# Optimization experiments

Hardware: AMD Instinct MI355X
Metric: run time of the kernel (lower is better)

## Reference

```python
import jax, jax.numpy as jnp
import numpy as np

D_MODEL = 1024
NUM_HEADS = 16
PERIOD_LEN = 4096
HEAD_DIM = D_MODEL // NUM_HEADS


def setup_inputs() -> dict:
    key = jax.random.key(0)
    ks = jax.random.split(key, 10)
    B, S, D = 2, 2048, D_MODEL
    scale = 1.0 / np.sqrt(D)
    inp = {
        "x": jax.random.normal(ks[0], (B, S, D), dtype=jnp.float32),
        "wq": jax.random.normal(ks[1], (D, D), dtype=jnp.float32) * scale,
        "bq": jnp.zeros((D,), dtype=jnp.float32),
        "wk": jax.random.normal(ks[2], (D, D), dtype=jnp.float32) * scale,
        "bk": jnp.zeros((D,), dtype=jnp.float32),
        "wv": jax.random.normal(ks[3], (D, D), dtype=jnp.float32) * scale,
        "bv": jnp.zeros((D,), dtype=jnp.float32),
        "wo": jax.random.normal(ks[4], (D, D), dtype=jnp.float32) * scale,
        "bo": jnp.zeros((D,), dtype=jnp.float32),
        # original init is zeros; use small randn so bias path is non-trivial
        "rel_bias": jax.random.normal(ks[5], (PERIOD_LEN, NUM_HEADS), dtype=jnp.float32) * 0.02,
    }
    return inp


def reference(x, wq, bq, wk, bk, wv, bv, wo, bo, rel_bias):
    B, S, D = x.shape
    H, Hd = NUM_HEADS, HEAD_DIM
    q = (x @ wq + bq).reshape(B, S, H, Hd).transpose(0, 2, 1, 3)  # [B,H,S,Hd]
    k = (x @ wk + bk).reshape(B, S, H, Hd).transpose(0, 2, 1, 3)
    v = (x @ wv + bv).reshape(B, S, H, Hd).transpose(0, 2, 1, 3)
    scores = jnp.einsum('bhqd,bhkd->bhqk', q, k) / jnp.sqrt(jnp.float32(Hd))
    if S <= PERIOD_LEN:
        pos = jnp.arange(S)
        circ = (pos[:, None] - pos[None, :]) % PERIOD_LEN  # [S,S]
        bias = rel_bias[circ]                               # [S,S,H]
        scores = scores + bias.transpose(2, 0, 1)[None]     # [1,H,S,S]
    attn = jax.nn.softmax(scores, axis=-1)
    out = jnp.einsum('bhqk,bhkd->bhqd', attn, v)
    out = out.transpose(0, 2, 1, 3).reshape(B, S, D)
    return out @ wo + bo
```

## Files before the change

kernel.cpp:

```cpp
#include <hip/hip_runtime.h>
#include <hip/hip_bf16.h>

#define D_MODEL 1024
#define NHEADS  16
#define HEADD   64
#define SEQ     2048
#define PERIOD  4096
#define LOG2E   1.44269504088896340736f

typedef __attribute__((ext_vector_type(4)))  float f32x4;
typedef __attribute__((ext_vector_type(16))) float f32x16;
typedef __attribute__((ext_vector_type(4)))  float fvec4;
typedef __attribute__((ext_vector_type(8)))  short s16x8;
typedef __attribute__((ext_vector_type(4)))  short s16x4;
typedef __attribute__((ext_vector_type(2)))  int   i32x2;
typedef __attribute__((ext_vector_type(4)))  int   i32x4;

__device__ __forceinline__ short bf16_bits(float f) {
    union { float f; unsigned u; } v; v.f = f;
    unsigned r = v.u + 0x7FFFu + ((v.u >> 16) & 1u);
    return (short)(r >> 16);
}

__device__ __forceinline__ int cvt_pk_bf16(float a, float b) {
    int r;
    asm("v_cvt_pk_bf16_f32 %0, %1, %2" : "=v"(r) : "v"(a), "v"(b));
    return r;
}

__device__ __forceinline__ float bf16_to_f32(short s) {
    return __int_as_float(((int)(unsigned short)s) << 16);
}

__device__ __forceinline__ float exp2_hw(float x) {
    float r;
    asm("v_exp_f32 %0, %1" : "=v"(r) : "v"(x));
    return r;
}

__device__ __forceinline__ void gload_lds16(const void* g, void* l) {
    __builtin_amdgcn_global_load_lds(
        (const __attribute__((address_space(1))) void*)g,
        (__attribute__((address_space(3))) void*)l, 16, 0, 0);
}

__global__ void cvt_x(const float* __restrict__ x, short* __restrict__ xb) {
    int i = blockIdx.x * blockDim.x + threadIdx.x;
    fvec4 v = ((const fvec4*)x)[i];
    s16x4 o;
    o.x = bf16_bits(v.x); o.y = bf16_bits(v.y);
    o.z = bf16_bits(v.z); o.w = bf16_bits(v.w);
    ((s16x4*)xb)[i] = o;
}

__global__ void transpose_w4(const float* __restrict__ wq, const float* __restrict__ wk,
                             const float* __restrict__ wv, const float* __restrict__ wo,
                             short* __restrict__ wqkv, short* __restrict__ wot) {
    __shared__ float tile[64][65];
    int wsel = blockIdx.y;
    const float* src = wsel == 0 ? wq : (wsel == 1 ? wk : (wsel == 2 ? wv : wo));
    short* dst = wsel < 3 ? wqkv + wsel * 1024 * 1024 : wot;
    int bx = blockIdx.x & 15, by = blockIdx.x >> 4;
    int n0 = bx * 64, k0 = by * 64;
    int t = threadIdx.x;
    int cr = t >> 4;
    int cc = (t & 15) * 4;
    for (int i = 0; i < 4; ++i) {
        int row = cr + i * 16;
        fvec4 v = *(const fvec4*)&src[(k0 + row) * D_MODEL + n0 + cc];
        tile[row][cc+0] = v.x; tile[row][cc+1] = v.y;
        tile[row][cc+2] = v.z; tile[row][cc+3] = v.w;
    }
    __syncthreads();
    for (int i = 0; i < 4; ++i) {
        int row = cr + i * 16;
        s16x4 o;
        o.x = bf16_bits(tile[cc+0][row]);
        o.y = bf16_bits(tile[cc+1][row]);
        o.z = bf16_bits(tile[cc+2][row]);
        o.w = bf16_bits(tile[cc+3][row]);
        *(s16x4*)&dst[(n0 + row) * D_MODEL + k0 + cc] = o;
    }
}

__global__ void transpose_v(const short* __restrict__ vb, short* __restrict__ vt) {
    __shared__ short tile[64][80];
    int bh = blockIdx.y, st = blockIdx.x;
    int b = bh >> 4, h = bh & 15;
    int s0 = st * 64;
    int t = threadIdx.x;
    int row = t >> 3, ch = t & 7;
    for (int i = 0; i < 2; ++i) {
        int r = row + i * 32;
        *(s16x8*)&tile[r][ch * 8] =
            *(const s16x8*)&vb[(b * SEQ + s0 + r) * D_MODEL + h * HEADD + ch * 8];
    }
    __syncthreads();
    for (int i = 0; i < 2; ++i) {
        int d = row + i * 32;
        s16x8 o;
        #pragma unroll
        for (int j = 0; j < 8; ++j) o[j] = tile[ch * 8 + j][d];
        *(s16x8*)&vt[(b * D_MODEL + h * HEADD + d) * SEQ + s0 + ch * 8] = o;
    }
}

__global__ void build_biasq(const float* __restrict__ rb, f32x4* __restrict__ bq4) {
    int id = blockIdx.x * 256 + threadIdx.x;
    int h = id >> 12, a = id & 4095;
    f32x4 v;
    #pragma unroll
    for (int j = 0; j < 4; ++j)
        v[j] = rb[((a + j) & (PERIOD - 1)) * NHEADS + h] * LOG2E - 16.0f;
    bq4[id] = v;
}

__global__ __launch_bounds__(256, 3) void gemm_qkv(
    const short* __restrict__ A, const short* __restrict__ Bt,
    const float* __restrict__ biasq, const float* __restrict__ biask,
    const float* __restrict__ biasv,
    short* __restrict__ qb, short* __restrict__ kb, short* __restrict__ vb)
{
    __shared__ short As[2][128 * 64];
    __shared__ short Bs[2][64 * 64];
    int tid = threadIdx.x;
    int lane = tid & 63, wid = tid >> 6;
    int ln = lane & 15, g = lane >> 4;
    int wr = (wid >> 1) * 64, wc = (wid & 1) * 32;

    int bid = blockIdx.x;
    int xcd = bid & 7, slot = bid >> 3;
    int mb = xcd * 4 + (slot / 48);
    int nb = slot % 48;
    int m0 = mb * 128, n0 = nb * 64;

    int wsel = n0 >> 10;
    const float* bias = wsel == 0 ? biasq : (wsel == 1 ? biask : biasv);
    short* dst = wsel == 0 ? qb : (wsel == 1 ? kb : vb);
    float osc = wsel == 0 ? (0.125f * LOG2E) : 1.0f;
    int ncol0 = n0 & 1023;

    f32x4 acc[4][2] = {};

    auto STAGE = [&](int kt, int bi) {
        #pragma unroll
        for (int i = 0; i < 4; ++i) {
            int idx = i * 256 + tid;
            int row = idx >> 3, ch = idx & 7;
            int gch = ch ^ (row & 7);
            gload_lds16(&A[(m0 + row) * 1024 + kt + gch * 8],
                        (char*)&As[bi][0] + (i * 256 + wid * 64) * 16);
        }
        #pragma unroll
        for (int i = 0; i < 2; ++i) {
            int idx = i * 256 + tid;
            int row = idx >> 3, ch = idx & 7;
            int gch = ch ^ (row & 7);
            gload_lds16(&Bt[(n0 + row) * 1024 + kt + gch * 8],
                        (char*)&Bs[bi][0] + (i * 256 + wid * 64) * 16);
        }
    };

    STAGE(0, 0);
    __syncthreads();

    for (int kt = 0; kt < 16; ++kt) {
        int bi = kt & 1;
        if (kt < 15) STAGE((kt + 1) * 64, bi ^ 1);

        s16x8 af[4][2], bfr[2][2];
        #pragma unroll
        for (int m = 0; m < 4; ++m) {
            int row = wr + m * 16 + ln;
            #pragma unroll
            for (int kc = 0; kc < 2; ++kc)
                af[m][kc] = *(const s16x8*)&As[bi][row * 64 + (((kc * 4 + g) ^ (row & 7)) * 8)];
        }
        #pragma unroll
        for (int n = 0; n < 2; ++n) {
            int row = wc + n * 16 + ln;
            #pragma unroll
            for (int kc = 0; kc < 2; ++kc)
                bfr[n][kc] = *(const s16x8*)&Bs[bi][row * 64 + (((kc * 4 + g) ^ (row & 7)) * 8)];
        }
        #pragma unroll
        for (int kc = 0; kc < 2; ++kc)
            #pragma unroll
            for (int m = 0; m < 4; ++m)
                #pragma unroll
                for (int n = 0; n < 2; ++n)
                    acc[m][n] = __builtin_amdgcn_mfma_f32_16x16x32_bf16(af[m][kc], bfr[n][kc], acc[m][n], 0, 0, 0);

        __syncthreads();
    }

    #pragma unroll
    for (int m = 0; m < 4; ++m) {
        int gr0 = m0 + wr + m * 16 + g * 4;
        #pragma unroll
        for (int n = 0; n < 2; ++n) {
            int gc = ncol0 + wc + n * 16 + ln;
            float bvv = bias[gc];
            #pragma unroll
            for (int r = 0; r < 4; ++r)
                dst[(gr0 + r) * 1024 + gc] = bf16_bits((acc[m][n][r] + bvv) * osc);
        }
    }
}

template<int MODE>
__global__ __launch_bounds__(256) void gemm_bias(
    const short* __restrict__ A, const short* __restrict__ Bt,
    const float* __restrict__ bias, void* __restrict__ Cout)
{
    __shared__ short As[2][128 * 64];
    __shared__ short Bs[2][64 * 64];
    int tid = threadIdx.x;
    int lane = tid & 63, wid = tid >> 6;
    int ln = lane & 15, g = lane >> 4;
    int wr = (wid >> 1) * 64, wc = (wid & 1) * 32;

    int bid = blockIdx.x;
    int xcd = bid & 7, slot = bid >> 3;
    int mb = xcd * 4 + (slot >> 4);
    int nb = slot & 15;
    int m0 = mb * 128, n0 = nb * 64;

    f32x4 acc[4][2] = {};

    auto STAGE = [&](int kt, int bi) {
        #pragma unroll
        for (int i = 0; i < 4; ++i) {
            int idx = i * 256 + tid;
            int row = idx >> 3, ch = idx & 7;
            int gch = ch ^ (row & 7);
            gload_lds16(&A[(m0 + row) * 1024 + kt + gch * 8],
                        (char*)&As[bi][0] + (i * 256 + wid * 64) * 16);
        }
        #pragma unroll
        for (int i = 0; i < 2; ++i) {
            int idx = i * 256 + tid;
            int row = idx >> 3, ch = idx & 7;
            int gch = ch ^ (row & 7);
            gload_lds16(&Bt[(n0 + row) * 1024 + kt + gch * 8],
                        (char*)&Bs[bi][0] + (i * 256 + wid * 64) * 16);
        }
    };

    STAGE(0, 0);
    __syncthreads();

    for (int kt = 0; kt < 16; ++kt) {
        int bi = kt & 1;
        if (kt < 15) STAGE((kt + 1) * 64, bi ^ 1);

        s16x8 af[4][2], bfr[2][2];
        #pragma unroll
        for (int m = 0; m < 4; ++m) {
            int row = wr + m * 16 + ln;
            #pragma unroll
            for (int kc = 0; kc < 2; ++kc)
                af[m][kc] = *(const s16x8*)&As[bi][row * 64 + (((kc * 4 + g) ^ (row & 7)) * 8)];
        }
        #pragma unroll
        for (int n = 0; n < 2; ++n) {
            int row = wc + n * 16 + ln;
            #pragma unroll
            for (int kc = 0; kc < 2; ++kc)
                bfr[n][kc] = *(const s16x8*)&Bs[bi][row * 64 + (((kc * 4 + g) ^ (row & 7)) * 8)];
        }
        #pragma unroll
        for (int kc = 0; kc < 2; ++kc)
            #pragma unroll
            for (int m = 0; m < 4; ++m)
                #pragma unroll
                for (int n = 0; n < 2; ++n)
                    acc[m][n] = __builtin_amdgcn_mfma_f32_16x16x32_bf16(af[m][kc], bfr[n][kc], acc[m][n], 0, 0, 0);

        __syncthreads();
    }

    #pragma unroll
    for (int m = 0; m < 4; ++m) {
        int gr0 = m0 + wr + m * 16 + g * 4;
        #pragma unroll
        for (int n = 0; n < 2; ++n) {
            int gc = n0 + wc + n * 16 + ln;
            float bv = bias[gc];
            #pragma unroll
            for (int r = 0; r < 4; ++r) {
                int gr = gr0 + r;
                float v = acc[m][n][r] + bv;
                if (MODE == 0)      ((short*)Cout)[gr * 1024 + gc] = bf16_bits(v * (0.125f * LOG2E));
                else if (MODE == 1) ((short*)Cout)[gr * 1024 + gc] = bf16_bits(v);
                else                ((float*)Cout)[gr * 1024 + gc] = v;
            }
        }
    }
}

__global__ __launch_bounds__(256, 2) void attn_partial(
    const short* __restrict__ qb,
    const short* __restrict__ kb,
    const short* __restrict__ vt,
    const f32x4* __restrict__ biasq,
    short* __restrict__ po,
    float* __restrict__ pl)
{
    __shared__ short KV[2][2][64 * 64];

    int tid = threadIdx.x;
    int lane = tid & 63;
    int wid = tid >> 6;
    int l31 = lane & 31, hi = lane >> 5;

    int bid = blockIdx.x;
    int xcd = bid & 7, slot = bid >> 3;
    int hb = xcd * 4 + (slot >> 5);
    int qt = (slot >> 1) & 15;
    int half = slot & 1;
    int h = hb & 15, b = hb >> 4;
    int q0 = qt * 128 + wid * 32;
    int qrow = q0 + l31;
    int kbase = half * 1024;

    s16x8 aq[4];
    #pragma unroll
    for (int kk = 0; kk < 4; ++kk)
        aq[kk] = *(const s16x8*)&qb[(b * SEQ + qrow) * D_MODEL + h * HEADD + kk * 16 + hi * 8];

    const f32x4* bq = biasq + h * PERIOD;

    float lrow = 0.f;
    f32x16 ot[2] = {};

    auto STAGE = [&](int k0, int bi) {
        #pragma unroll
        for (int i = 0; i < 2; ++i) {
            int idx = i * 256 + tid;
            int row = idx >> 3, ch = idx & 7;
            int gch = ch ^ ((row & 7) ^ ((row >> 3) & 3));
            gload_lds16(&kb[(b * SEQ + k0 + row) * D_MODEL + h * HEADD + gch * 8],
                        (char*)&KV[bi][0][0] + (i * 256 + wid * 64) * 16);
            gload_lds16(&vt[(b * D_MODEL + h * HEADD + row) * SEQ + k0 + gch * 8],
                        (char*)&KV[bi][1][0] + (i * 256 + wid * 64) * 16);
        }
    };

    STAGE(kbase, 0);
    __syncthreads();

    for (int kt = 0; kt < 16; ++kt) {
        int k0 = kbase + kt * 64;
        int bi = kt & 1;
        if (kt < 15) STAGE(k0 + 64, bi ^ 1);

        f32x4 bv[2][4];
        #pragma unroll
        for (int kt32 = 0; kt32 < 2; ++kt32)
            #pragma unroll
            for (int rq = 0; rq < 4; ++rq) {
                int kq = k0 + kt32 * 32 + rq * 8 + hi * 4;
                bv[kt32][rq] = bq[(qrow - kq - 3) & (PERIOD - 1)];
            }

        f32x16 s[2];
        const short* Ksp = &KV[bi][0][0];
        const short* Vsp = &KV[bi][1][0];
        __builtin_amdgcn_s_setprio(1);
        #pragma unroll
        for (int kt32 = 0; kt32 < 2; ++kt32) {
            f32x16 acc = {};
            int rowK = kt32 * 32 + l31;
            int swz = (rowK & 7) ^ ((rowK >> 3) & 3);
            #pragma unroll
            for (int kk = 0; kk < 4; ++kk) {
                s16x8 kf = *(const s16x8*)&Ksp[rowK * 64 + (((2 * kk + hi) ^ swz) * 8)];
                acc = __builtin_amdgcn_mfma_f32_32x32x16_bf16(kf, aq[kk], acc, 0, 0, 0);
            }
            s[kt32] = acc;
        }
        __builtin_amdgcn_s_setprio(0);

        #pragma unroll
        for (int kt32 = 0; kt32 < 2; ++kt32)
            #pragma unroll
            for (int rq = 0; rq < 4; ++rq) {
                s[kt32][rq * 4 + 0] = exp2_hw(s[kt32][rq * 4 + 0] + bv[kt32][rq][3]);
                s[kt32][rq * 4 + 1] = exp2_hw(s[kt32][rq * 4 + 1] + bv[kt32][rq][2]);
                s[kt32][rq * 4 + 2] = exp2_hw(s[kt32][rq * 4 + 2] + bv[kt32][rq][1]);
                s[kt32][rq * 4 + 3] = exp2_hw(s[kt32][rq * 4 + 3] + bv[kt32][rq][0]);
            }

        float sm[16];
        #pragma unroll
        for (int t = 0; t < 16; ++t) sm[t] = s[0][t] + s[1][t];
        #pragma unroll
        for (int t = 0; t < 8; ++t) sm[t] += sm[t + 8];
        #pragma unroll
        for (int t = 0; t < 4; ++t) sm[t] += sm[t + 4];
        float psum = (sm[0] + sm[1]) + (sm[2] + sm[3]);
        {
            i32x2 r = __builtin_amdgcn_permlane32_swap(__float_as_int(psum), __float_as_int(psum), false, false);
            psum = __int_as_float(r[0]) + __int_as_float(r[1]);
        }
        lrow += psum;

        #pragma unroll
        for (int kt32 = 0; kt32 < 2; ++kt32) {
            int pk[8];
            #pragma unroll
            for (int i = 0; i < 8; ++i)
                pk[i] = cvt_pk_bf16(s[kt32][2 * i], s[kt32][2 * i + 1]);
            #pragma unroll
            for (int ks = 0; ks < 2; ++ks) {
                int a0 = pk[ks * 4 + 0], a1 = pk[ks * 4 + 1];
                int b0 = pk[ks * 4 + 2], b1 = pk[ks * 4 + 3];
                i32x2 r0 = __builtin_amdgcn_permlane32_swap(a0, b0, false, false);
                i32x2 r1 = __builtin_amdgcn_permlane32_swap(a1, b1, false, false);
                i32x4 wi;
                wi[0] = r0[0];
                wi[1] = r1[0];
                wi[2] = r0[1];
                wi[3] = r1[1];
                s16x8 pb = __builtin_bit_cast(s16x8, wi);
                __builtin_amdgcn_s_setprio(1);
                #pragma unroll
                for (int dd = 0; dd < 2; ++dd) {
                    int rowV = dd * 32 + l31;
                    int swzV = (rowV & 7) ^ ((rowV >> 3) & 3);
                    int chV = kt32 * 4 + ks * 2 + hi;
                    s16x8 vf = *(const s16x8*)&Vsp[rowV * 64 + ((chV ^ swzV) * 8)];
                    ot[dd] = __builtin_amdgcn_mfma_f32_32x32x16_bf16(vf, pb, ot[dd], 0, 0, 0);
                }
                __builtin_amdgcn_s_setprio(0);
            }
        }

        __syncthreads();
    }

    short* poH = po + half * (4096 * 1024);
    int obase = (b * SEQ + qrow) * D_MODEL + h * HEADD;
    #pragma unroll
    for (int dd = 0; dd < 2; ++dd)
        #pragma unroll
        for (int rq = 0; rq < 4; ++rq) {
            i32x2 st;
            st[0] = cvt_pk_bf16(ot[dd][rq * 4 + 0], ot[dd][rq * 4 + 1]);
            st[1] = cvt_pk_bf16(ot[dd][rq * 4 + 2], ot[dd][rq * 4 + 3]);
            *(i32x2*)&poH[obase + dd * 32 + rq * 8 + hi * 4] = st;
        }
    if (hi == 0)
        pl[half * (4096 * 16) + (b * SEQ + qrow) * 16 + h] = lrow;
}

__global__ __launch_bounds__(256) void attn_merge(
    const short* __restrict__ po, const float* __restrict__ pl,
    short* __restrict__ ao)
{
    int idx = blockIdx.x * 256 + threadIdx.x;
    int base = idx * 8;
    int row = base >> 10, col = base & 1023, h = col >> 6;
    float l = pl[row * 16 + h] + pl[4096 * 16 + row * 16 + h];
    float inv = 1.0f / l;
    s16x8 a = *(const s16x8*)&po[row * 1024 + col];
    s16x8 c = *(const s16x8*)&po[4096 * 1024 + row * 1024 + col];
    float v[8];
    #pragma unroll
    for (int j = 0; j < 8; ++j)
        v[j] = (bf16_to_f32(a[j]) + bf16_to_f32(c[j])) * inv;
    i32x4 o;
    o[0] = cvt_pk_bf16(v[0], v[1]);
    o[1] = cvt_pk_bf16(v[2], v[3]);
    o[2] = cvt_pk_bf16(v[4], v[5]);
    o[3] = cvt_pk_bf16(v[6], v[7]);
    *(i32x4*)&ao[base] = o;
}

extern "C" void kernel_launch(void* const* d_in, const int* in_sizes, int n_in,
                              void* d_out, int out_size, void* d_ws, size_t ws_size,
                              hipStream_t stream) {
    const float* x  = (const float*)d_in[0];
    const float* wq = (const float*)d_in[1];
    const float* bq = (const float*)d_in[2];
    const float* wk = (const float*)d_in[3];
    const float* bk = (const float*)d_in[4];
    const float* wv = (const float*)d_in[5];
    const float* bv = (const float*)d_in[6];
    const float* wo = (const float*)d_in[7];
    const float* bo = (const float*)d_in[8];
    const float* rb = (const float*)d_in[9];

    char* ws = (char*)d_ws;
    short* xb   = (short*)(ws);
    short* wqkv = (short*)(ws + (8u  << 20));
    short* wot  = (short*)(ws + (14u << 20));
    short* qb   = (short*)(ws + (16u << 20));
    short* kb   = (short*)(ws + (24u << 20));
    short* vb   = (short*)(ws + (32u << 20));
    short* vt   = (short*)(ws + (40u << 20));
    f32x4* bqt  = (f32x4*)(ws + (32u << 20));
    short* po   = (short*)(ws + (48u << 20));
    float* pl   = (float*)(ws + (64u << 20));
    short* ao   = xb;

    cvt_x<<<4096, 256, 0, stream>>>(x, xb);
    transpose_w4<<<dim3(256, 4), 256, 0, stream>>>(wq, wk, wv, wo, wqkv, wot);

    gemm_qkv<<<1536, 256, 0, stream>>>(xb, wqkv, bq, bk, bv, qb, kb, vb);
    transpose_v<<<dim3(32, 32), 256, 0, stream>>>(vb, vt);
    build_biasq<<<256, 256, 0, stream>>>(rb, bqt);

    attn_partial<<<1024, 256, 0, stream>>>(qb, kb, vt, bqt, po, pl);
    attn_merge<<<2048, 256, 0, stream>>>(po, pl, ao);

    gemm_bias<3><<<512, 256, 0, stream>>>(ao, wot, bo, (float*)d_out);
}
```

Before: 134.0 us.

## Merge prep kernels into one launch and write V transposed from QKV GEMM

Folds the x conversion, the weight transposes and the rel-bias table build into a single block-indexed prep kernel, removing three separate launches. The QKV GEMM epilogue now writes V directly in transposed [B, D, S] layout with packed bf16 stores, which removes the transpose_v kernel and its extra round trip through memory. The transposed V stores are 8-byte writes strided by sequence length, so they may coalesce less well than the row-major stores. The bias table now lives in the workspace slot that V used to occupy.

Measured after the change: 127.3 us. 1.05x faster.

```diff
diff --git a/kernel.cpp b/kernel.cpp
--- a/kernel.cpp
+++ b/kernel.cpp
@@ -44,82 +44,64 @@
         (__attribute__((address_space(3))) void*)l, 16, 0, 0);
 }
 
-__global__ void cvt_x(const float* __restrict__ x, short* __restrict__ xb) {
-    int i = blockIdx.x * blockDim.x + threadIdx.x;
-    fvec4 v = ((const fvec4*)x)[i];
-    s16x4 o;
-    o.x = bf16_bits(v.x); o.y = bf16_bits(v.y);
-    o.z = bf16_bits(v.z); o.w = bf16_bits(v.w);
-    ((s16x4*)xb)[i] = o;
-}
-
-__global__ void transpose_w4(const float* __restrict__ wq, const float* __restrict__ wk,
-                             const float* __restrict__ wv, const float* __restrict__ wo,
-                             short* __restrict__ wqkv, short* __restrict__ wot) {
+__global__ void prep_all(const float* __restrict__ x,
+                         const float* __restrict__ wq, const float* __restrict__ wk,
+                         const float* __restrict__ wv, const float* __restrict__ wo,
+                         const float* __restrict__ rb,
+                         short* __restrict__ xb, short* __restrict__ wqkv,
+                         short* __restrict__ wot, f32x4* __restrict__ bq4) {
     __shared__ float tile[64][65];
-    int wsel = blockIdx.y;
-    const float* src = wsel == 0 ? wq : (wsel == 1 ? wk : (wsel == 2 ? wv : wo));
-    short* dst = wsel < 3 ? wqkv + wsel * 1024 * 1024 : wot;
-    int bx = blockIdx.x & 15, by = blockIdx.x >> 4;
-    int n0 = bx * 64, k0 = by * 64;
+    int bid = blockIdx.x;
     int t = threadIdx.x;
-    int cr = t >> 4;
-    int cc = (t & 15) * 4;
-    for (int i = 0; i < 4; ++i) {
-        int row = cr + i * 16;
-        fvec4 v = *(const fvec4*)&src[(k0 + row) * D_MODEL + n0 + cc];
-        tile[row][cc+0] = v.x; tile[row][cc+1] = v.y;
-        tile[row][cc+2] = v.z; tile[row][cc+3] = v.w;
+    if (bid < 4096) {
+        int i = bid * 256 + t;
+        fvec4 v = ((const fvec4*)x)[i];
+        s16x4 o;
+        o.x = bf16_bits(v.x); o.y = bf16_bits(v.y);
+        o.z = bf16_bits(v.z); o.w = bf16_bits(v.w);
+        ((s16x4*)xb)[i] = o;
+    } else if (bid < 5120) {
+        int b2 = bid - 4096;
+        int wsel = b2 >> 8;
+        int bxy = b2 & 255;
+        const float* src = wsel == 0 ? wq : (wsel == 1 ? wk : (wsel == 2 ? wv : wo));
+        short* dst = wsel < 3 ? wqkv + wsel * 1024 * 1024 : wot;
+        int bx = bxy & 15, by = bxy >> 4;
+        int n0 = bx * 64, k0 = by * 64;
+        int cr = t >> 4;
+        int cc = (t & 15) * 4;
+        for (int i = 0; i < 4; ++i) {
+            int row = cr + i * 16;
+            fvec4 v = *(const fvec4*)&src[(k0 + row) * D_MODEL + n0 + cc];
+            tile[row][cc+0] = v.x; tile[row][cc+1] = v.y;
+            tile[row][cc+2] = v.z; tile[row][cc+3] = v.w;
+        }
+        __syncthreads();
+        for (int i = 0; i < 4; ++i) {
+            int row = cr + i * 16;
+            s16x4 o;
+            o.x = bf16_bits(tile[cc+0][row]);
+            o.y = bf16_bits(tile[cc+1][row]);
+            o.z = bf16_bits(tile[cc+2][row]);
+            o.w = bf16_bits(tile[cc+3][row]);
+            *(s16x4*)&dst[(n0 + row) * D_MODEL + k0 + cc] = o;
+        }
+    } else {
+        int id = (bid - 5120) * 256 + t;
+        int h = id >> 12, a = id & 4095;
+        f32x4 v;
+        #pragma unroll
+        for (int j = 0; j < 4; ++j)
+            v[j] = rb[((a + j) & (PERIOD - 1)) * NHEADS + h] * LOG2E - 16.0f;
+        bq4[id] = v;
     }
-    __syncthreads();
-    for (int i = 0; i < 4; ++i) {
-        int row = cr + i * 16;
-        s16x4 o;
-        o.x = bf16_bits(tile[cc+0][row]);
-        o.y = bf16_bits(tile[cc+1][row]);
-        o.z = bf16_bits(tile[cc+2][row]);
-        o.w = bf16_bits(tile[cc+3][row]);
-        *(s16x4*)&dst[(n0 + row) * D_MODEL + k0 + cc] = o;
-    }
-}
-
-__global__ void transpose_v(const short* __restrict__ vb, short* __restrict__ vt) {
-    __shared__ short tile[64][80];
-    int bh = blockIdx.y, st = blockIdx.x;
-    int b = bh >> 4, h = bh & 15;
-    int s0 = st * 64;
-    int t = threadIdx.x;
-    int row = t >> 3, ch = t & 7;
-    for (int i = 0; i < 2; ++i) {
-        int r = row + i * 32;
-        *(s16x8*)&tile[r][ch * 8] =
-            *(const s16x8*)&vb[(b * SEQ + s0 + r) * D_MODEL + h * HEADD + ch * 8];
-    }
-    __syncthreads();
-    for (int i = 0; i < 2; ++i) {
-        int d = row + i * 32;
-        s16x8 o;
-        #pragma unroll
-        for (int j = 0; j < 8; ++j) o[j] = tile[ch * 8 + j][d];
-        *(s16x8*)&vt[(b * D_MODEL + h * HEADD + d) * SEQ + s0 + ch * 8] = o;
-    }
-}
-
-__global__ void build_biasq(const float* __restrict__ rb, f32x4* __restrict__ bq4) {
-    int id = blockIdx.x * 256 + threadIdx.x;
-    int h = id >> 12, a = id & 4095;
-    f32x4 v;
-    #pragma unroll
-    for (int j = 0; j < 4; ++j)
-        v[j] = rb[((a + j) & (PERIOD - 1)) * NHEADS + h] * LOG2E - 16.0f;
-    bq4[id] = v;
 }
 
 __global__ __launch_bounds__(256, 3) void gemm_qkv(
     const short* __restrict__ A, const short* __restrict__ Bt,
     const float* __restrict__ biasq, const float* __restrict__ biask,
     const float* __restrict__ biasv,
-    short* __restrict__ qb, short* __restrict__ kb, short* __restrict__ vb)
+    short* __restrict__ qb, short* __restrict__ kb, short* __restrict__ vt)
 {
     __shared__ short As[2][128 * 64];
     __shared__ short Bs[2][64 * 64];
@@ -136,7 +118,6 @@
 
     int wsel = n0 >> 10;
     const float* bias = wsel == 0 ? biasq : (wsel == 1 ? biask : biasv);
-    short* dst = wsel == 0 ? qb : (wsel == 1 ? kb : vb);
     float osc = wsel == 0 ? (0.125f * LOG2E) : 1.0f;
     int ncol0 = n0 & 1023;
 
@@ -194,16 +175,34 @@
         __syncthreads();
     }
 
-    #pragma unroll
-    for (int m = 0; m < 4; ++m) {
-        int gr0 = m0 + wr + m * 16 + g * 4;
-        #pragma unroll
-        for (int n = 0; n < 2; ++n) {
-            int gc = ncol0 + wc + n * 16 + ln;
-            float bvv = bias[gc];
-            #pragma unroll
-            for (int r = 0; r < 4; ++r)
-                dst[(gr0 + r) * 1024 + gc] = bf16_bits((acc[m][n][r] + bvv) * osc);
+    if (wsel == 2) {
+        #pragma unroll
+        for (int m = 0; m < 4; ++m) {
+            int gr0 = m0 + wr + m * 16 + g * 4;
+            int b = gr0 >> 11, s0 = gr0 & 2047;
+            #pragma unroll
+            for (int n = 0; n < 2; ++n) {
+                int gc = ncol0 + wc + n * 16 + ln;
+                float bvv = bias[gc];
+                i32x2 st;
+                st[0] = cvt_pk_bf16(acc[m][n][0] + bvv, acc[m][n][1] + bvv);
+                st[1] = cvt_pk_bf16(acc[m][n][2] + bvv, acc[m][n][3] + bvv);
+                *(i32x2*)&vt[(b * 1024 + gc) * 2048 + s0] = st;
+            }
+        }
+    } else {
+        short* dst = wsel == 0 ? qb : kb;
+        #pragma unroll
+        for (int m = 0; m < 4; ++m) {
+            int gr0 = m0 + wr + m * 16 + g * 4;
+            #pragma unroll
+            for (int n = 0; n < 2; ++n) {
+                int gc = ncol0 + wc + n * 16 + ln;
+                float bvv = bias[gc];
+                #pragma unroll
+                for (int r = 0; r < 4; ++r)
+                    dst[(gr0 + r) * 1024 + gc] = bf16_bits((acc[m][n][r] + bvv) * osc);
+            }
         }
     }
 }
@@ -498,19 +497,15 @@
     short* wot  = (short*)(ws + (14u << 20));
     short* qb   = (short*)(ws + (16u << 20));
     short* kb   = (short*)(ws + (24u << 20));
-    short* vb   = (short*)(ws + (32u << 20));
+    f32x4* bqt  = (f32x4*)(ws + (32u << 20));
     short* vt   = (short*)(ws + (40u << 20));
-    f32x4* bqt  = (f32x4*)(ws + (32u << 20));
     short* po   = (short*)(ws + (48u << 20));
     float* pl   = (float*)(ws + (64u << 20));
     short* ao   = xb;
 
-    cvt_x<<<4096, 256, 0, stream>>>(x, xb);
-    transpose_w4<<<dim3(256, 4), 256, 0, stream>>>(wq, wk, wv, wo, wqkv, wot);
-
-    gemm_qkv<<<1536, 256, 0, stream>>>(xb, wqkv, bq, bk, bv, qb, kb, vb);
-    transpose_v<<<dim3(32, 32), 256, 0, stream>>>(vb, vt);
-    build_biasq<<<256, 256, 0, stream>>>(rb, bqt);
+    prep_all<<<5376, 256, 0, stream>>>(x, wq, wk, wv, wo, rb, xb, wqkv, wot, bqt);
+
+    gemm_qkv<<<1536, 256, 0, stream>>>(xb, wqkv, bq, bk, bv, qb, kb, vt);
 
     attn_partial<<<1024, 256, 0, stream>>>(qb, kb, vt, bqt, po, pl);
     attn_merge<<<2048, 256, 0, stream>>>(po, pl, ao);
```
